# Optimization experiments

Measured on AMD Instinct MI355X. Metric: run time of the kernel, lower is better.

## Reference

```python
import jax, jax.numpy as jnp
import numpy as np

CODEBOOK_SIZE = 8192
TOKEN_SIZE = 256
COMMITMENT_COST = 0.25


def setup_inputs() -> dict:
    key = jax.random.key(0)
    k1, k2 = jax.random.split(key)
    z = jax.random.normal(k1, (32, 1024, TOKEN_SIZE), dtype=jnp.float32)
    # embedding initialized uniform in [-1/K, 1/K] as in torch module
    embedding = jax.random.uniform(
        k2, (CODEBOOK_SIZE, TOKEN_SIZE), dtype=jnp.float32,
        minval=-1.0 / CODEBOOK_SIZE, maxval=1.0 / CODEBOOK_SIZE)
    return {"z": z, "embedding": embedding}


def reference(z, embedding):
    B, T, D = z.shape
    zf = z.reshape(B * T, D)                               # [N, D]
    # squared euclidean distances: ||z||^2 + ||e||^2 - 2 z.e
    d = (jnp.sum(zf * zf, axis=1, keepdims=True)
         + jnp.sum(embedding * embedding, axis=1)
         - 2.0 * jnp.einsum('nd,kd->nk', zf, embedding))   # [N, K]
    idx = jnp.argmin(d, axis=1)                            # [N]
    z_q = embedding[idx].reshape(B, T, D)                  # codebook gather
    commitment_loss = COMMITMENT_COST * jnp.mean(
        (jax.lax.stop_gradient(z_q) - z) ** 2)
    codebook_loss = jnp.mean((z_q - jax.lax.stop_gradient(z)) ** 2)
    loss = commitment_loss + codebook_loss                 # ema_update=False
    # straight-through estimator
    z_q_st = z + jax.lax.stop_gradient(z_q - z)
    return (z_q_st, loss, commitment_loss, codebook_loss,
            idx.reshape(B, T))
```

## Files before the change

kernel.cpp:

```cpp
#include <hip/hip_runtime.h>
#include <hip/hip_bf16.h>
#include <cfloat>

#define N_TOK   32768
#define K_CODES 8192
#define D_DIM   256
#define BTOK    128
#define CHUNK   128
#define NSPLIT  4
#define SPLITK  (K_CODES / NSPLIT)
#define CTAU_M  3.0e-5f
#define CAND_MM 2.4e-5f
#define MAXCAND 16
#define RBTOK   32
#define NRS     8
#define RSPLIT  (K_CODES / NRS)

typedef __attribute__((ext_vector_type(4)))  short bf16x4;
typedef __attribute__((ext_vector_type(8)))  short bf16x8;
typedef __attribute__((ext_vector_type(16))) float f32x16;


__device__ __forceinline__ float np_sumsq256(const float* __restrict__ row) {
    #pragma clang fp contract(off)
    float blk[2];
    #pragma unroll
    for (int b = 0; b < 2; b++) {
        const float* x = row + b * 128;
        float r[8];
        #pragma unroll
        for (int j = 0; j < 8; j++) { float v = x[j]; r[j] = v * v; }
        for (int i = 8; i < 128; i += 8) {
            #pragma unroll
            for (int j = 0; j < 8; j++) { float v = x[i + j]; r[j] += v * v; }
        }
        blk[b] = ((r[0] + r[1]) + (r[2] + r[3])) + ((r[4] + r[5]) + (r[6] + r[7]));
    }
    return blk[0] + blk[1];
}

__device__ __forceinline__ float np_einsum256(const float* __restrict__ a,
                                              const float* __restrict__ b) {
    #pragma clang fp contract(off)
    float A0 = 0.f, A1 = 0.f, A2 = 0.f, A3 = 0.f;
    for (int m = 0; m < 256; m += 16) {
        A0 = a[m+ 0]*b[m+ 0] + (a[m+ 4]*b[m+ 4] + (a[m+ 8]*b[m+ 8] + (a[m+12]*b[m+12] + A0)));
        A1 = a[m+ 1]*b[m+ 1] + (a[m+ 5]*b[m+ 5] + (a[m+ 9]*b[m+ 9] + (a[m+13]*b[m+13] + A1)));
        A2 = a[m+ 2]*b[m+ 2] + (a[m+ 6]*b[m+ 6] + (a[m+10]*b[m+10] + (a[m+14]*b[m+14] + A2)));
        A3 = a[m+ 3]*b[m+ 3] + (a[m+ 7]*b[m+ 7] + (a[m+11]*b[m+11] + (a[m+15]*b[m+15] + A3)));
    }
    return (A0 + A1) + (A2 + A3);
}

__device__ __forceinline__ float np_dtilde(float Cn, float e2k, float g) {
    #pragma clang fp contract(off)
    float t = Cn + e2k;
    float d = t - 2.0f * g;
    return d;
}

__device__ __forceinline__ unsigned short bf16_rne(float f) {
    unsigned u = __float_as_uint(f);
    unsigned r = u + 0x7fffu + ((u >> 16) & 1u);
    return (unsigned short)(r >> 16);
}
__device__ __forceinline__ void split_bf16(float f, short& hi, short& lo) {
    unsigned short h = bf16_rne(f);
    hi = (short)h;
    float hf = __uint_as_float(((unsigned)h) << 16);
    lo = (short)bf16_rne(f - hf);
}
__device__ __forceinline__ void split8v(float4 a, float4 b, bf16x8& h, bf16x8& l) {
    float f[8] = {a.x, a.y, a.z, a.w, b.x, b.y, b.z, b.w};
    #pragma unroll
    for (int i = 0; i < 8; i += 2) {
        __hip_bfloat162 hp = __float22bfloat162_rn(make_float2(f[i], f[i + 1]));
        unsigned hu; __builtin_memcpy(&hu, &hp, 4);
        h[i]     = (short)(hu & 0xffffu);
        h[i + 1] = (short)(hu >> 16);
        float h0 = __uint_as_float(hu << 16);
        float h1 = __uint_as_float(hu & 0xffff0000u);
        __hip_bfloat162 lp = __float22bfloat162_rn(make_float2(f[i] - h0, f[i + 1] - h1));
        unsigned lu; __builtin_memcpy(&lu, &lp, 4);
        l[i]     = (short)(lu & 0xffffu);
        l[i + 1] = (short)(lu >> 16);
    }
}

#define MFMA3(A, ah, al, bh, bl) \
    A = __builtin_amdgcn_mfma_f32_32x32x16_bf16(ah, bh, A, 0, 0, 0); \
    A = __builtin_amdgcn_mfma_f32_32x32x16_bf16(ah, bl, A, 0, 0, 0); \
    A = __builtin_amdgcn_mfma_f32_32x32x16_bf16(al, bh, A, 0, 0, 0);

__global__ __launch_bounds__(256) void prep_e_kernel(
    const float* __restrict__ emb, float* __restrict__ e2np,
    float* __restrict__ e2h, unsigned* __restrict__ ccount,
    double* __restrict__ loss_sum)
{
    int k = blockIdx.x * 256 + threadIdx.x;
    float v = np_sumsq256(emb + (size_t)k * D_DIM);
    e2np[k] = v;
    e2h[k]  = 0.5f * v;
    if (k == 0) { *ccount = 0u; *loss_sum = 0.0; }
}

__global__ __launch_bounds__(256) void prep_z_kernel(
    const float* __restrict__ z, float* __restrict__ Cnp)
{
    int t = blockIdx.x * 256 + threadIdx.x;
    Cnp[t] = np_sumsq256(z + (size_t)t * D_DIM);
}

__global__ __launch_bounds__(256) void cvt_e_kernel(
    const float* __restrict__ src, short* __restrict__ hi, short* __restrict__ lo)
{
    size_t p = ((size_t)blockIdx.x * 256 + threadIdx.x) * 8;
    float4 v0 = *(const float4*)(src + p);
    float4 v1 = *(const float4*)(src + p + 4);
    short h[8], l[8];
    split_bf16(v0.x, h[0], l[0]); split_bf16(v0.y, h[1], l[1]);
    split_bf16(v0.z, h[2], l[2]); split_bf16(v0.w, h[3], l[3]);
    split_bf16(v1.x, h[4], l[4]); split_bf16(v1.y, h[5], l[5]);
    split_bf16(v1.z, h[6], l[6]); split_bf16(v1.w, h[7], l[7]);
    bf16x8 vh = {h[0],h[1],h[2],h[3],h[4],h[5],h[6],h[7]};
    bf16x8 vl = {l[0],l[1],l[2],l[3],l[4],l[5],l[6],l[7]};
    *(bf16x8*)(hi + p) = vh;
    *(bf16x8*)(lo + p) = vl;
}

#define B_ESH 0
#define B_ESL 4096
#define B_ZSH 8192
#define B_ZSL 12288
#define TILE1 1024

__global__ __launch_bounds__(512, 4) void bulk_kernel(
    const float* __restrict__ zf,
    const short* __restrict__ ehi, const short* __restrict__ elo,
    const float* __restrict__ e2h,
    float* __restrict__ m1a, float* __restrict__ m2a, int* __restrict__ i1a)
{
    __shared__ __align__(16) short smem[2][16384];
    __shared__ float e2sall[SPLITK];
    __shared__ float s1m[BTOK], s2m[BTOK];
    __shared__ int   i1m[BTOK];

    const int tid  = threadIdx.x;
    const int lane = tid & 63;
    const int w    = tid >> 6;
    const int wt   = w & 1;
    const int wc   = w >> 1;
    const int g     = blockIdx.x & 255;
    const int split = blockIdx.x >> 8;
    const int tok0  = g * BTOK;
    const int cs0   = split * SPLITK;

    const int r0 = tid >> 2, q0 = tid & 3;
    const int so0 = r0 * 32 + ((q0 ^ ((r0 >> 1) & 3)) << 3);

    const int l31 = lane & 31, hh = lane >> 5;
    const int swz = (l31 >> 1) & 3;
    const int arow = (wc * 32 + l31) * 32;
    const int brow = (wt * 64 + l31) * 32;
    const int a0 = arow + ((hh ^ swz) << 3);
    const int a1 = arow + (((2 + hh) ^ swz) << 3);
    const int b0 = brow + ((hh ^ swz) << 3);
    const int b1 = brow + (((2 + hh) ^ swz) << 3);

    float m1[2] = {-FLT_MAX, -FLT_MAX}, m2[2] = {-FLT_MAX, -FLT_MAX};
    int   k1[2] = {0x7fffffff, 0x7fffffff};

    bf16x8 ehA, elA;  float4 zfaA, zfbA;
    bf16x8 ehB, elB;  float4 zfaB, zfbB;

    f32x16 acc[2];
    #pragma unroll
    for (int j = 0; j < 2; j++)
        #pragma unroll
        for (int r = 0; r < 16; r++) acc[j][r] = 0.f;

    const int NST = (SPLITK / CHUNK) * 8;

    auto ISSUE_A = [&](int s) {
        const int code0 = cs0 + (s >> 3) * CHUNK;
        const int d0 = (s & 7) * 32;
        const size_t ei = ((size_t)(code0 + r0) << 8) + d0 + (q0 << 3);
        const size_t zi = ((size_t)(tok0 + r0) << 8) + d0 + (q0 << 3);
        ehA = *(const bf16x8*)(ehi + ei);
        elA = *(const bf16x8*)(elo + ei);
        zfaA = *(const float4*)(zf + zi);
        zfbA = *(const float4*)(zf + zi + 4);
    };
    auto ISSUE_B = [&](int s) {
        const int code0 = cs0 + (s >> 3) * CHUNK;
        const int d0 = (s & 7) * 32;
        const size_t ei = ((size_t)(code0 + r0) << 8) + d0 + (q0 << 3);
        const size_t zi = ((size_t)(tok0 + r0) << 8) + d0 + (q0 << 3);
        ehB = *(const bf16x8*)(ehi + ei);
        elB = *(const bf16x8*)(elo + ei);
        zfaB = *(const float4*)(zf + zi);
        zfbB = *(const float4*)(zf + zi + 4);
    };

    auto STORE_A = [&](int buf) {
        bf16x8 zh, zl;
        split8v(zfaA, zfbA, zh, zl);
        short* sm = smem[buf];
        *(bf16x8*)(sm + B_ESH + so0) = ehA;
        *(bf16x8*)(sm + B_ESL + so0) = elA;
        *(bf16x8*)(sm + B_ZSH + so0) = zh;
        *(bf16x8*)(sm + B_ZSL + so0) = zl;
    };
    auto STORE_B = [&](int buf) {
        bf16x8 zh, zl;
        split8v(zfaB, zfbB, zh, zl);
        short* sm = smem[buf];
        *(bf16x8*)(sm + B_ESH + so0) = ehB;
        *(bf16x8*)(sm + B_ESL + so0) = elB;
        *(bf16x8*)(sm + B_ZSH + so0) = zh;
        *(bf16x8*)(sm + B_ZSL + so0) = zl;
    };

    #pragma unroll
    for (int i = 0; i < SPLITK / 512; i++) {
        int idx = tid + i * 512;
        e2sall[idx] = e2h[cs0 + idx];
    }
    ISSUE_A(0);
    ISSUE_B(1);
    STORE_A(0);
    __syncthreads();

    #pragma unroll 2
    for (int s = 0; s < NST; s++) {
        const int cur = s & 1;
        if (s + 2 < NST) {
            if (cur == 0) ISSUE_A(s + 2); else ISSUE_B(s + 2);
        }
        {
            const short* sm = smem[cur];
            {
                bf16x8 ah  = *(const bf16x8*)(sm + B_ESH + a0);
                bf16x8 al  = *(const bf16x8*)(sm + B_ESL + a0);
                bf16x8 b0h = *(const bf16x8*)(sm + B_ZSH + b0);
                bf16x8 b0l = *(const bf16x8*)(sm + B_ZSL + b0);
                bf16x8 b1h = *(const bf16x8*)(sm + B_ZSH + TILE1 + b0);
                bf16x8 b1l = *(const bf16x8*)(sm + B_ZSL + TILE1 + b0);
                MFMA3(acc[0], ah, al, b0h, b0l);
                MFMA3(acc[1], ah, al, b1h, b1l);
            }
            {
                bf16x8 ah  = *(const bf16x8*)(sm + B_ESH + a1);
                bf16x8 al  = *(const bf16x8*)(sm + B_ESL + a1);
                bf16x8 b0h = *(const bf16x8*)(sm + B_ZSH + b1);
                bf16x8 b0l = *(const bf16x8*)(sm + B_ZSL + b1);
                bf16x8 b1h = *(const bf16x8*)(sm + B_ZSH + TILE1 + b1);
                bf16x8 b1l = *(const bf16x8*)(sm + B_ZSL + TILE1 + b1);
                MFMA3(acc[0], ah, al, b0h, b0l);
                MFMA3(acc[1], ah, al, b1h, b1l);
            }
        }
        if ((s & 7) == 7) {
            const int code0 = cs0 + (s >> 3) * CHUNK;
            const float* e2c = e2sall + (s >> 3) * CHUNK;
            float ev[16];
            #pragma unroll
            for (int r = 0; r < 16; r++)
                ev[r] = e2c[wc * 32 + hh * 4 + (r & 3) + ((r >> 2) << 3)];
            #pragma unroll
            for (int tt = 0; tt < 2; tt++) {
                #pragma unroll
                for (int r = 0; r < 16; r++) {
                    float a = acc[tt][r] - ev[r];
                    int code = code0 + wc * 32 + hh * 4 + (r & 3) + ((r >> 2) << 3);
                    if (a > m1[tt]) { m2[tt] = m1[tt]; m1[tt] = a; k1[tt] = code; }
                    else if (a > m2[tt]) m2[tt] = a;
                }
            }
            #pragma unroll
            for (int j = 0; j < 2; j++)
                #pragma unroll
                for (int r = 0; r < 16; r++) acc[j][r] = 0.f;
        }
        if (s + 1 < NST) {
            if (cur == 0) STORE_B(cur ^ 1); else STORE_A(cur ^ 1);
        }
        asm volatile("s_waitcnt lgkmcnt(0)" ::: "memory");
        __builtin_amdgcn_s_barrier();
        __builtin_amdgcn_sched_barrier(0);
    }

    #pragma unroll
    for (int tt = 0; tt < 2; tt++) {
        float o1 = __shfl_xor(m1[tt], 32);
        float o2 = __shfl_xor(m2[tt], 32);
        int   oi = __shfl_xor(k1[tt], 32);
        bool take = (o1 > m1[tt]) || (o1 == m1[tt] && oi < k1[tt]);
        float w1 = take ? o1 : m1[tt];
        int   wi = take ? oi : k1[tt];
        float ls = take ? m1[tt] : o1;
        m2[tt] = fmaxf(fmaxf(m2[tt], o2), ls);
        m1[tt] = w1; k1[tt] = wi;
    }
    __syncthreads();
    if (wc == 0 && lane < 32) {
        #pragma unroll
        for (int tt = 0; tt < 2; tt++) {
            int tl = wt * 64 + tt * 32 + lane;
            s1m[tl] = m1[tt]; s2m[tl] = m2[tt]; i1m[tl] = k1[tt];
        }
    }
    __syncthreads();
    #pragma unroll
    for (int mw = 1; mw < 3; mw++) {
        if (wc == mw && lane < 32) {
            #pragma unroll
            for (int tt = 0; tt < 2; tt++) {
                int tl = wt * 64 + tt * 32 + lane;
                float a1 = s1m[tl], a2 = s2m[tl]; int ai = i1m[tl];
                bool take = (a1 > m1[tt]) || (a1 == m1[tt] && ai < k1[tt]);
                float w1 = take ? a1 : m1[tt];
                int   wi = take ? ai : k1[tt];
                float ls = take ? m1[tt] : a1;
                float w2 = fmaxf(fmaxf(m2[tt], a2), ls);
                s1m[tl] = w1; s2m[tl] = w2; i1m[tl] = wi;
            }
        }
        __syncthreads();
    }
    if (wc == 3 && lane < 32) {
        #pragma unroll
        for (int tt = 0; tt < 2; tt++) {
            int tl = wt * 64 + tt * 32 + lane;
            float a1 = s1m[tl], a2 = s2m[tl]; int ai = i1m[tl];
            bool take = (a1 > m1[tt]) || (a1 == m1[tt] && ai < k1[tt]);
            float w1 = take ? a1 : m1[tt];
            int   wi = take ? ai : k1[tt];
            float ls = take ? m1[tt] : a1;
            float w2 = fmaxf(fmaxf(m2[tt], a2), ls);
            size_t t = (size_t)(tok0 + tl) * NSPLIT + split;
            m1a[t] = w1; m2a[t] = w2; i1a[t] = wi;
        }
    }
}

__global__ __launch_bounds__(256) void merge_kernel(
    const float* __restrict__ m1a, const float* __restrict__ m2a,
    const int* __restrict__ i1a, float* __restrict__ m1f,
    int* __restrict__ idxf, int* __restrict__ clist,
    unsigned* __restrict__ ccount, unsigned* __restrict__ ccnt_g)
{
    int t = blockIdx.x * 256 + threadIdx.x;
    ccnt_g[t] = 0u;
    float w1 = m1a[t * NSPLIT], w2 = m2a[t * NSPLIT];
    int   wi = i1a[t * NSPLIT];
    #pragma unroll
    for (int s = 1; s < NSPLIT; s++) {
        float a1 = m1a[t * NSPLIT + s], a2 = m2a[t * NSPLIT + s];
        int   ai = i1a[t * NSPLIT + s];
        bool take = (a1 > w1) || (a1 == w1 && ai < wi);
        float n1 = take ? a1 : w1;
        int   ni = take ? ai : wi;
        float ls = take ? w1 : a1;
        w2 = fmaxf(fmaxf(w2, a2), ls);
        w1 = n1; wi = ni;
    }
    idxf[t] = wi; m1f[t] = w1;
    if (w1 - w2 < CTAU_M) {
        unsigned p = atomicAdd(ccount, 1u);
        clist[p] = t;
    }
}

#define R_ESH 0
#define R_ESL 4096
#define R_ZSH 8192
#define R_ZSL 9216

__global__ __launch_bounds__(256) void rescue_kernel(
    const float* __restrict__ zf,
    const short* __restrict__ ehi, const short* __restrict__ elo,
    const float* __restrict__ e2h, const float* __restrict__ m1f,
    const unsigned* __restrict__ ccount, const int* __restrict__ clist,
    unsigned* __restrict__ ccnt_g, int* __restrict__ cand_g)
{
    const unsigned count = *ccount;
    const unsigned base  = blockIdx.x * RBTOK;
    if (base >= count) return;
    const int nt = min(RBTOK, (int)(count - base));
    const int sp = blockIdx.y;

    __shared__ __align__(16) short rsm[10240];
    __shared__ int   tls[RBTOK];
    __shared__ float thr[RBTOK];
    __shared__ float e2s[CHUNK];

    const int tid  = threadIdx.x;
    const int lane = tid & 63;
    const int w    = tid >> 6;

    if (tid < RBTOK) {
        int s = (tid < nt) ? tid : (nt - 1);
        int t = clist[base + s];
        tls[tid] = t;
        thr[tid] = (tid < nt) ? (m1f[t] - CAND_MM) : FLT_MAX;
    }
    __syncthreads();

    const int l31 = lane & 31, hh = lane >> 5;
    const float mythr = thr[l31];
    const int   mytok = tls[l31];
    const int swz = (l31 >> 1) & 3;
    const int arow = (w * 32 + l31) * 32;
    const int brow = l31 * 32;
    const int a0 = arow + ((hh ^ swz) << 3);
    const int a1 = arow + (((2 + hh) ^ swz) << 3);
    const int b0 = brow + ((hh ^ swz) << 3);
    const int b1 = brow + (((2 + hh) ^ swz) << 3);

    const int er0 = tid >> 2, eq0 = tid & 3;
    const int er1 = er0 + 64;
    const int eso0 = er0 * 32 + ((eq0 ^ ((er0 >> 1) & 3)) << 3);
    const int eso1 = er1 * 32 + ((eq0 ^ ((er1 >> 1) & 3)) << 3);
    const int zr = (tid & 127) >> 2, zq = tid & 3;
    const int zso = zr * 32 + ((zq ^ ((zr >> 1) & 3)) << 3);

    for (int c = 0; c < RSPLIT / CHUNK; c++) {
        const int code0 = sp * RSPLIT + c * CHUNK;
        const float e2v = (tid < CHUNK) ? e2h[code0 + tid] : 0.f;
        f32x16 acc;
        #pragma unroll
        for (int r = 0; r < 16; r++) acc[r] = 0.f;

        for (int st = 0; st < 8; st++) {
            const int d0 = st * 32;
            const size_t ei0 = ((size_t)(code0 + er0) << 8) + d0 + (eq0 << 3);
            const size_t ei1 = ((size_t)(code0 + er1) << 8) + d0 + (eq0 << 3);
            bf16x8 eh0 = *(const bf16x8*)(ehi + ei0);
            bf16x8 el0 = *(const bf16x8*)(elo + ei0);
            bf16x8 eh1 = *(const bf16x8*)(ehi + ei1);
            bf16x8 el1 = *(const bf16x8*)(elo + ei1);
            bf16x8 zh = {}, zl = {};
            if (tid < 128) {
                const size_t zi = ((size_t)tls[zr] << 8) + d0 + (zq << 3);
                float4 za = *(const float4*)(zf + zi);
                float4 zb = *(const float4*)(zf + zi + 4);
                split8v(za, zb, zh, zl);
            }
            __syncthreads();
            *(bf16x8*)(rsm + R_ESH + eso0) = eh0;
            *(bf16x8*)(rsm + R_ESL + eso0) = el0;
            *(bf16x8*)(rsm + R_ESH + eso1) = eh1;
            *(bf16x8*)(rsm + R_ESL + eso1) = el1;
            if (tid < 128) {
                *(bf16x8*)(rsm + R_ZSH + zso) = zh;
                *(bf16x8*)(rsm + R_ZSL + zso) = zl;
            }
            if (st == 0 && tid < CHUNK) e2s[tid] = e2v;
            __syncthreads();
            {
                bf16x8 ah = *(const bf16x8*)(rsm + R_ESH + a0);
                bf16x8 al = *(const bf16x8*)(rsm + R_ESL + a0);
                bf16x8 bh = *(const bf16x8*)(rsm + R_ZSH + b0);
                bf16x8 bl = *(const bf16x8*)(rsm + R_ZSL + b0);
                MFMA3(acc, ah, al, bh, bl);
            }
            {
                bf16x8 ah = *(const bf16x8*)(rsm + R_ESH + a1);
                bf16x8 al = *(const bf16x8*)(rsm + R_ESL + a1);
                bf16x8 bh = *(const bf16x8*)(rsm + R_ZSH + b1);
                bf16x8 bl = *(const bf16x8*)(rsm + R_ZSL + b1);
                MFMA3(acc, ah, al, bh, bl);
            }
        }
        #pragma unroll
        for (int r = 0; r < 16; r++) {
            const int local = w * 32 + hh * 4 + (r & 3) + ((r >> 2) << 3);
            float a = acc[r] - e2s[local];
            if (a >= mythr) {
                unsigned p = atomicAdd(&ccnt_g[mytok], 1u);
                if (p < MAXCAND) cand_g[(size_t)mytok * MAXCAND + p] = code0 + local;
            }
        }
    }
}

__global__ __launch_bounds__(256) void resolve_kernel(
    const float* __restrict__ z, const float* __restrict__ emb,
    const float* __restrict__ e2np, const float* __restrict__ Cnp,
    const unsigned* __restrict__ ccount, const int* __restrict__ clist,
    const unsigned* __restrict__ ccnt_g, const int* __restrict__ cand_g,
    int* __restrict__ idxf)
{
    const unsigned count = *ccount;
    const int lane = threadIdx.x & 63;
    const int w    = threadIdx.x >> 6;
    for (unsigned c = blockIdx.x * 4 + w; c < count; c += gridDim.x * 4) {
        const int t = clist[c];
        const int n = (int)min(ccnt_g[t], (unsigned)MAXCAND);
        float bd = FLT_MAX; int bk = 0x7fffffff;
        if (lane < n) {
            const int k = cand_g[(size_t)t * MAXCAND + lane];
            float g = np_einsum256(z + (size_t)t * D_DIM, emb + (size_t)k * D_DIM);
            bd = np_dtilde(Cnp[t], e2np[k], g);
            bk = k;
        }
        #pragma unroll
        for (int off = 32; off >= 1; off >>= 1) {
            float od = __shfl_xor(bd, off);
            int   ok = __shfl_xor(bk, off);
            if (od < bd || (od == bd && ok < bk)) { bd = od; bk = ok; }
        }
        if (lane == 0 && n > 0) idxf[t] = bk;
    }
}

__global__ __launch_bounds__(256) void out_loss_kernel(
    const float* __restrict__ z, const float* __restrict__ emb,
    const int* __restrict__ idxf, float* __restrict__ out0,
    double* __restrict__ loss_sum)
{
    const int total4 = N_TOK * (D_DIM / 4);
    double lsum = 0.0;
    for (int p = blockIdx.x * 256 + threadIdx.x; p < total4; p += gridDim.x * 256) {
        const int n  = p >> 6;
        const int d4 = p & 63;
        const int k  = idxf[n];
        float4 zv = ((const float4*)z)[p];
        float4 ev = ((const float4*)(emb + (size_t)k * D_DIM))[d4];
        float dx = ev.x - zv.x, dy = ev.y - zv.y,
              dz = ev.z - zv.z, dw = ev.w - zv.w;
        float4 o;
        o.x = zv.x + dx; o.y = zv.y + dy; o.z = zv.z + dz; o.w = zv.w + dw;
        ((float4*)out0)[p] = o;
        lsum += (double)dx * dx + (double)dy * dy
              + (double)dz * dz + (double)dw * dw;
    }
    #pragma unroll
    for (int off = 32; off >= 1; off >>= 1) lsum += __shfl_xor(lsum, off);
    __shared__ double wsum[4];
    const int wv = threadIdx.x >> 6;
    if ((threadIdx.x & 63) == 0) wsum[wv] = lsum;
    __syncthreads();
    if (threadIdx.x == 0)
        atomicAdd(loss_sum, wsum[0] + wsum[1] + wsum[2] + wsum[3]);
}

__global__ __launch_bounds__(256) void finalize_kernel(
    const int* __restrict__ idxf, const double* __restrict__ loss_sum,
    float* __restrict__ out)
{
    const int t = blockIdx.x * 256 + threadIdx.x;
    if (t < N_TOK) out[8388611 + t] = (float)idxf[t];
    if (t == 0) {
        double mse = *loss_sum * (1.0 / 8388608.0);
        out[8388608] = (float)(1.25 * mse);
        out[8388609] = (float)(0.25 * mse);
        out[8388610] = (float)mse;
    }
}

extern "C" void kernel_launch(void* const* d_in, const int* in_sizes, int n_in,
                              void* d_out, int out_size, void* d_ws, size_t ws_size,
                              hipStream_t stream)
{
    const float* z   = (const float*)d_in[0];
    const float* emb = (const float*)d_in[1];
    float* out = (float*)d_out;
    char*  ws  = (char*)d_ws;
    char*  ob  = (char*)d_out;

    short*    ehi    = (short*)(ob + 0);
    short*    elo    = (short*)(ob + 4194304);
    float*    m1a    = (float*)(ob + 8388608);
    float*    m2a    = (float*)(ob + 8912896);
    int*      i1a    = (int*)(ob + 9437184);
    int*      cand_g = (int*)(ob + 9961472);

    double*   loss_sum = (double*)(ws + 0);
    unsigned* ccount   = (unsigned*)(ws + 8);
    float*    e2np     = (float*)(ws + 16);
    float*    e2h      = (float*)(ws + 32784);
    float*    Cnp      = (float*)(ws + 65552);
    float*    m1f      = (float*)(ws + 196624);
    int*      idxf     = (int*)(ws + 327696);
    int*      clist    = (int*)(ws + 458768);
    unsigned* ccnt_g   = (unsigned*)(ws + 589840);

    prep_e_kernel<<<dim3(K_CODES / 256), dim3(256), 0, stream>>>(
        emb, e2np, e2h, ccount, loss_sum);
    prep_z_kernel<<<dim3(N_TOK / 256), dim3(256), 0, stream>>>(z, Cnp);
    cvt_e_kernel<<<dim3(K_CODES * D_DIM / 8 / 256), dim3(256), 0, stream>>>(emb, ehi, elo);
    bulk_kernel<<<dim3((N_TOK / BTOK) * NSPLIT), dim3(512), 0, stream>>>(
        z, ehi, elo, e2h, m1a, m2a, i1a);
    merge_kernel<<<dim3(N_TOK / 256), dim3(256), 0, stream>>>(
        m1a, m2a, i1a, m1f, idxf, clist, ccount, ccnt_g);
    rescue_kernel<<<dim3(N_TOK / RBTOK, NRS), dim3(256), 0, stream>>>(
        z, ehi, elo, e2h, m1f, ccount, clist, ccnt_g, cand_g);
    resolve_kernel<<<dim3(128), dim3(256), 0, stream>>>(
        z, emb, e2np, Cnp, ccount, clist, ccnt_g, cand_g, idxf);
    out_loss_kernel<<<dim3(1024), dim3(256), 0, stream>>>(
        z, emb, idxf, out, loss_sum);
    finalize_kernel<<<dim3(N_TOK / 256), dim3(256), 0, stream>>>(
        idxf, loss_sum, out);
}
```

Measured before the change: 760.3 us.

## Use single-bf16 MFMA in bulk pass with wider candidate margins

The bulk distance pass switches from a three-term split-bf16 product (hi*hi + hi*lo + lo*hi) to a single bf16 hi*hi MFMA. This drops the lo arrays from shared memory and global loads and cuts the MFMA count per tile by a factor of three. The candidate thresholds are widened to absorb the larger bf16 error, so more tokens fall through to the exact rescue/resolve path. The code split also goes from 4 to 3 uneven chunks (22/21/21) so the grid fits with occupancy raised to 6, at the cost of more work in the fallback stages.

```diff
diff --git a/kernel.cpp b/kernel.cpp
--- a/kernel.cpp
+++ b/kernel.cpp
@@ -7,10 +7,9 @@
 #define D_DIM   256
 #define BTOK    128
 #define CHUNK   128
-#define NSPLIT  4
-#define SPLITK  (K_CODES / NSPLIT)
-#define CTAU_M  3.0e-5f
-#define CAND_MM 2.4e-5f
+#define NSPLIT  3
+#define CTAU_M  1.1e-4f
+#define CAND_MM 6.0e-5f
 #define MAXCAND 16
 #define RBTOK   32
 #define NRS     8
@@ -85,6 +84,18 @@
         l[i]     = (short)(lu & 0xffffu);
         l[i + 1] = (short)(lu >> 16);
     }
+}
+__device__ __forceinline__ bf16x8 cvt8h(float4 a, float4 b) {
+    float f[8] = {a.x, a.y, a.z, a.w, b.x, b.y, b.z, b.w};
+    bf16x8 h;
+    #pragma unroll
+    for (int i = 0; i < 8; i += 2) {
+        __hip_bfloat162 hp = __float22bfloat162_rn(make_float2(f[i], f[i + 1]));
+        unsigned hu; __builtin_memcpy(&hu, &hp, 4);
+        h[i]     = (short)(hu & 0xffffu);
+        h[i + 1] = (short)(hu >> 16);
+    }
+    return h;
 }
 
 #define MFMA3(A, ah, al, bh, bl) \
@@ -129,19 +140,16 @@
 }
 
 #define B_ESH 0
-#define B_ESL 4096
-#define B_ZSH 8192
-#define B_ZSL 12288
+#define B_ZSH 4096
 #define TILE1 1024
 
-__global__ __launch_bounds__(512, 4) void bulk_kernel(
+__global__ __launch_bounds__(512, 6) void bulk_kernel(
     const float* __restrict__ zf,
-    const short* __restrict__ ehi, const short* __restrict__ elo,
-    const float* __restrict__ e2h,
+    const short* __restrict__ ehi, const float* __restrict__ e2h,
     float* __restrict__ m1a, float* __restrict__ m2a, int* __restrict__ i1a)
 {
-    __shared__ __align__(16) short smem[2][16384];
-    __shared__ float e2sall[SPLITK];
+    __shared__ __align__(16) short smem[2][8192];
+    __shared__ float e2sall[22 * CHUNK];
     __shared__ float s1m[BTOK], s2m[BTOK];
     __shared__ int   i1m[BTOK];
 
@@ -153,7 +161,9 @@
     const int g     = blockIdx.x & 255;
     const int split = blockIdx.x >> 8;
     const int tok0  = g * BTOK;
-    const int cs0   = split * SPLITK;
+    const int cbase = split * 21 + (split ? 1 : 0);
+    const int nch   = split ? 21 : 22;
+    const int cs0   = cbase * CHUNK;
 
     const int r0 = tid >> 2, q0 = tid & 3;
     const int so0 = r0 * 32 + ((q0 ^ ((r0 >> 1) & 3)) << 3);
@@ -170,8 +180,8 @@
     float m1[2] = {-FLT_MAX, -FLT_MAX}, m2[2] = {-FLT_MAX, -FLT_MAX};
     int   k1[2] = {0x7fffffff, 0x7fffffff};
 
-    bf16x8 ehA, elA;  float4 zfaA, zfbA;
-    bf16x8 ehB, elB;  float4 zfaB, zfbB;
+    bf16x8 ehA;  float4 zfaA, zfbA;
+    bf16x8 ehB;  float4 zfaB, zfbB;
 
     f32x16 acc[2];
     #pragma unroll
@@ -179,7 +189,7 @@
         #pragma unroll
         for (int r = 0; r < 16; r++) acc[j][r] = 0.f;
 
-    const int NST = (SPLITK / CHUNK) * 8;
+    const int NST = nch * 8;
 
     auto ISSUE_A = [&](int s) {
         const int code0 = cs0 + (s >> 3) * CHUNK;
@@ -187,7 +197,6 @@
         const size_t ei = ((size_t)(code0 + r0) << 8) + d0 + (q0 << 3);
         const size_t zi = ((size_t)(tok0 + r0) << 8) + d0 + (q0 << 3);
         ehA = *(const bf16x8*)(ehi + ei);
-        elA = *(const bf16x8*)(elo + ei);
         zfaA = *(const float4*)(zf + zi);
         zfbA = *(const float4*)(zf + zi + 4);
     };
@@ -197,35 +206,25 @@
         const size_t ei = ((size_t)(code0 + r0) << 8) + d0 + (q0 << 3);
         const size_t zi = ((size_t)(tok0 + r0) << 8) + d0 + (q0 << 3);
         ehB = *(const bf16x8*)(ehi + ei);
-        elB = *(const bf16x8*)(elo + ei);
         zfaB = *(const float4*)(zf + zi);
         zfbB = *(const float4*)(zf + zi + 4);
     };
 
     auto STORE_A = [&](int buf) {
-        bf16x8 zh, zl;
-        split8v(zfaA, zfbA, zh, zl);
+        bf16x8 zh = cvt8h(zfaA, zfbA);
         short* sm = smem[buf];
         *(bf16x8*)(sm + B_ESH + so0) = ehA;
-        *(bf16x8*)(sm + B_ESL + so0) = elA;
         *(bf16x8*)(sm + B_ZSH + so0) = zh;
-        *(bf16x8*)(sm + B_ZSL + so0) = zl;
     };
     auto STORE_B = [&](int buf) {
-        bf16x8 zh, zl;
-        split8v(zfaB, zfbB, zh, zl);
+        bf16x8 zh = cvt8h(zfaB, zfbB);
         short* sm = smem[buf];
         *(bf16x8*)(sm + B_ESH + so0) = ehB;
-        *(bf16x8*)(sm + B_ESL + so0) = elB;
         *(bf16x8*)(sm + B_ZSH + so0) = zh;
-        *(bf16x8*)(sm + B_ZSL + so0) = zl;
     };
 
-    #pragma unroll
-    for (int i = 0; i < SPLITK / 512; i++) {
-        int idx = tid + i * 512;
+    for (int idx = tid; idx < nch * CHUNK; idx += 512)
         e2sall[idx] = e2h[cs0 + idx];
-    }
     ISSUE_A(0);
     ISSUE_B(1);
     STORE_A(0);
@@ -241,23 +240,17 @@
             const short* sm = smem[cur];
             {
                 bf16x8 ah  = *(const bf16x8*)(sm + B_ESH + a0);
-                bf16x8 al  = *(const bf16x8*)(sm + B_ESL + a0);
                 bf16x8 b0h = *(const bf16x8*)(sm + B_ZSH + b0);
-                bf16x8 b0l = *(const bf16x8*)(sm + B_ZSL + b0);
                 bf16x8 b1h = *(const bf16x8*)(sm + B_ZSH + TILE1 + b0);
-                bf16x8 b1l = *(const bf16x8*)(sm + B_ZSL + TILE1 + b0);
-                MFMA3(acc[0], ah, al, b0h, b0l);
-                MFMA3(acc[1], ah, al, b1h, b1l);
+                acc[0] = __builtin_amdgcn_mfma_f32_32x32x16_bf16(ah, b0h, acc[0], 0, 0, 0);
+                acc[1] = __builtin_amdgcn_mfma_f32_32x32x16_bf16(ah, b1h, acc[1], 0, 0, 0);
             }
             {
                 bf16x8 ah  = *(const bf16x8*)(sm + B_ESH + a1);
-                bf16x8 al  = *(const bf16x8*)(sm + B_ESL + a1);
                 bf16x8 b0h = *(const bf16x8*)(sm + B_ZSH + b1);
-                bf16x8 b0l = *(const bf16x8*)(sm + B_ZSL + b1);
                 bf16x8 b1h = *(const bf16x8*)(sm + B_ZSH + TILE1 + b1);
-                bf16x8 b1l = *(const bf16x8*)(sm + B_ZSL + TILE1 + b1);
-                MFMA3(acc[0], ah, al, b0h, b0l);
-                MFMA3(acc[1], ah, al, b1h, b1l);
+                acc[0] = __builtin_amdgcn_mfma_f32_32x32x16_bf16(ah, b0h, acc[0], 0, 0, 0);
+                acc[1] = __builtin_amdgcn_mfma_f32_32x32x16_bf16(ah, b1h, acc[1], 0, 0, 0);
             }
         }
         if ((s & 7) == 7) {
@@ -592,7 +585,7 @@
     prep_z_kernel<<<dim3(N_TOK / 256), dim3(256), 0, stream>>>(z, Cnp);
     cvt_e_kernel<<<dim3(K_CODES * D_DIM / 8 / 256), dim3(256), 0, stream>>>(emb, ehi, elo);
     bulk_kernel<<<dim3((N_TOK / BTOK) * NSPLIT), dim3(512), 0, stream>>>(
-        z, ehi, elo, e2h, m1a, m2a, i1a);
+        z, ehi, e2h, m1a, m2a, i1a);
     merge_kernel<<<dim3(N_TOK / 256), dim3(256), 0, stream>>>(
         m1a, m2a, i1a, m1f, idxf, clist, ccount, ccnt_g);
     rescue_kernel<<<dim3(N_TOK / RBTOK, NRS), dim3(256), 0, stream>>>(
```

Measured after the change: 1.328 ms. +74.7%, slower.
